# Kernel tuning notes

Measured on AMD Instinct MI355X. Metric: run time of the kernel, lower is better.

## Reference

```python
import jax, jax.numpy as jnp
import numpy as np

N = 8192        # num_nodes == args.input_size (code ties them together)
H = 64          # hidden_size
E = 262144      # num edges (avg degree 32)
FIN = N + H     # GCNConv in_channels = input_size + hidden_size


def _glorot(key, shape):
    fan_in, fan_out = shape
    lim = np.sqrt(6.0 / (fan_in + fan_out)).astype(np.float32)
    return jax.random.uniform(key, shape, jnp.float32, -lim, lim)


def gcn_conv(x, W, b, src, dst, n):
    """PyG GCNConv: lin -> add self-loops -> sym-normalized scatter-add -> +bias."""
    h = x @ W                                   # [n, out]
    loop = jnp.arange(n, dtype=src.dtype)
    s = jnp.concatenate([src, loop])            # [E+n]
    d = jnp.concatenate([dst, loop])
    deg = jax.ops.segment_sum(jnp.ones(s.shape[0], h.dtype), d, num_segments=n)
    dinv = jnp.where(deg > 0, jax.lax.rsqrt(deg), 0.0)
    norm = dinv[s] * dinv[d]                    # [E+n]
    out = jax.ops.segment_sum(h[s] * norm[:, None], d, num_segments=n)
    return out + b


def setup_inputs() -> dict:
    key = jax.random.key(0)
    k1, k2, k3, k4, k5 = jax.random.split(key, 5)
    x = jax.random.normal(k1, (N, N), jnp.float32)
    hidden_state = jax.random.normal(k2, (N, H), jnp.float32)
    W1 = _glorot(k3, (FIN, 2 * H))
    b1 = jnp.ones((2 * H,), jnp.float32)        # reset_parameters: constant_(bias, 1.0)
    W2 = _glorot(k4, (FIN, H))
    b2 = jnp.zeros((H,), jnp.float32)           # PyG default bias init = zeros
    edge_index = jax.random.randint(k5, (2, E), 0, N, jnp.int32)
    return {"x": x, "hidden_state": hidden_state, "W1": W1, "b1": b1,
            "W2": W2, "b2": b2, "edge_index": edge_index}


def reference(x, hidden_state, W1, b1, W2, b2, edge_index):
    src, dst = edge_index[0], edge_index[1]
    ru_input = jnp.concatenate([x, hidden_state], axis=1)        # [N, N+H]
    ru = jax.nn.sigmoid(gcn_conv(ru_input, W1, b1, src, dst, N))  # [N, 2H]
    flat = ru.reshape(-1, N * 2 * H)                              # [1, N*2H]
    r = flat[:, : N * H].reshape(-1, H)                           # [N, H]
    u = flat[:, N * H :].reshape(-1, H)                           # [N, H]
    c_input = jnp.concatenate([x, r * hidden_state], axis=1)
    c = jnp.tanh(gcn_conv(c_input, W2, b2, src, dst, N))          # [N, H]
    new_hidden_state = u * hidden_state + (1.0 - u) * c
    return new_hidden_state
```

## Files before the change

### kernel.cpp

```cpp
#include <hip/hip_runtime.h>
#include <hip/hip_bf16.h>
#include <stdint.h>

typedef __bf16 bf16x8 __attribute__((ext_vector_type(8)));
typedef float  f32x4  __attribute__((ext_vector_type(4)));
typedef unsigned uint4v __attribute__((ext_vector_type(4)));
using bf16 = __hip_bfloat16;

#define NNODES 8192
#define FIN    8256
#define NCOL   192
#define KT32   258

enum : size_t {
  WCT_OFF  = 0,
  CNT_OFF  = 3170304,
  OFF_OFF  = 3203072,
  CUR_OFF  = 3236096,
  DNV_OFF  = 3268864,
  CSR_OFF  = 3301632,
  H1_OFF   = 4350208,
  HX2_OFF  = 8544512,
  RU_OFF   = 10641664,
  H2_OFF   = 14835968,
  YP_OFF   = 16933120,
  YP_SLICE = 6291456
};

__global__ void k_zero_i(int* p, int n) {
  int i = blockIdx.x * 256 + threadIdx.x;
  if (i < n) p[i] = 0;
}

__global__ void k_out_zero(float* out) {
  int i = blockIdx.x * 256 + threadIdx.x;
  if (i < NNODES * 64) out[i] = 0.f;
}

__global__ void k_prep_wctf(const float* __restrict__ W1, const float* __restrict__ W2,
                            bf16* __restrict__ wctf) {
  int gid = blockIdx.x * 256 + threadIdx.x;
  if (gid >= KT32 * 12 * 64) return;
  int t = gid / 768;
  int rem = gid - t * 768;
  int nf = rem >> 6, lane = rem & 63;
  int col = nf * 16 + (lane & 15);
  int k0 = t * 32 + (lane >> 4) * 8;
  union { bf16 h[8]; uint4 v; } u;
#pragma unroll
  for (int j = 0; j < 8; ++j) {
    int k = k0 + j;
    float v;
    if (col < 128)      v = W1[(size_t)k * 128 + col];
    else if (k < 8192)  v = W2[(size_t)k * 64 + (col - 128)];
    else                v = 0.f;
    u.h[j] = __float2bfloat16(v);
  }
  *(uint4*)(wctf + (size_t)gid * 8) = u.v;
}

__global__ void k_hist(const int* __restrict__ ei, int E, int* cnt) {
  int e = blockIdx.x * 256 + threadIdx.x;
  if (e < E) atomicAdd(&cnt[ei[E + e]], 1);
}

__global__ void k_scan(const int* __restrict__ cnt, int* __restrict__ offs,
                       int* __restrict__ cur, float* __restrict__ dinv) {
  __shared__ int part[256];
  int tid = threadIdx.x;
  int base = tid * 32;
  int s = 0;
#pragma unroll
  for (int j = 0; j < 32; j++) s += cnt[base + j];
  part[tid] = s;
  __syncthreads();
  for (int off = 1; off < 256; off <<= 1) {
    int a = (tid >= off) ? part[tid - off] : 0;
    __syncthreads();
    part[tid] += a;
    __syncthreads();
  }
  int run = (tid == 0) ? 0 : part[tid - 1];
  for (int j = 0; j < 32; j++) {
    int c = cnt[base + j];
    offs[base + j] = run;
    cur[base + j]  = run;
    dinv[base + j] = rsqrtf((float)(c + 1));
    run += c;
  }
  if (tid == 255) offs[NNODES] = run;
}

__global__ void k_fill(const int* __restrict__ ei, int E, int* cur, int* __restrict__ csr) {
  int e = blockIdx.x * 256 + threadIdx.x;
  if (e < E) {
    int d = ei[E + e];
    int p = atomicAdd(&cur[d], 1);
    csr[p] = ei[e];
  }
}

__device__ __forceinline__ bf16x8 pack8(float4 a, float4 b) {
  union { bf16 h[8]; bf16x8 v; } u;
  u.h[0] = __float2bfloat16(a.x); u.h[1] = __float2bfloat16(a.y);
  u.h[2] = __float2bfloat16(a.z); u.h[3] = __float2bfloat16(a.w);
  u.h[4] = __float2bfloat16(b.x); u.h[5] = __float2bfloat16(b.y);
  u.h[6] = __float2bfloat16(b.z); u.h[7] = __float2bfloat16(b.w);
  return u.v;
}

union F4 { uint4v u; float4 f; bf16x8 h; };

__device__ __forceinline__ void gld16(void* ldsdst, const void* gsrc) {
  __builtin_amdgcn_global_load_lds(
      (__attribute__((address_space(1))) void*)gsrc,
      (__attribute__((address_space(3))) void*)ldsdst, 16, 0, 0);
}

__global__ __launch_bounds__(64, 1) void k_gemm(const float* __restrict__ x,
                                                const float* __restrict__ hid,
                                                const bf16* __restrict__ wctf,
                                                float* __restrict__ yp,
                                                bf16* __restrict__ h1d,
                                                float* __restrict__ hx2d,
                                                int tpc) {
  __shared__ __align__(1024) unsigned char smem[36864];
  const int lane = threadIdx.x & 63;
  const int rl = lane & 15, g = lane >> 4;
  const int m0 = blockIdx.x * 32;
  const int chunk = blockIdx.y;
  const int t_lo = chunk * tpc;
  const int t_hi = (t_lo + tpc > KT32) ? KT32 : (t_lo + tpc);
  const int nt = t_hi - t_lo;
  if (nt <= 0) return;

  const float* asx[4]; const float* ash[4];
#pragma unroll
  for (int q = 0; q < 4; ++q) {
    int i = q * 64 + lane, row = i >> 3, s = i & 7;
    int sel = (s ^ (row & 7)) << 2;
    asx[q] = x + (size_t)(m0 + row) * 8192 + sel;
    ash[q] = hid + (size_t)(m0 + row) * 64 + sel;
  }
  const bf16* bsrc = wctf + (size_t)lane * 8;

#define STAGE_A(buf, t) do {                                                   \
    const int _t = (t);                                                        \
    unsigned _d = (unsigned)(buf) * 4096u;                                     \
    if (_t < 256) {                                                            \
      const int _k = _t * 32;                                                  \
      _Pragma("unroll")                                                        \
      for (int q = 0; q < 4; ++q)                                              \
        gld16(smem + _d + (unsigned)(q * 64 + lane) * 16u, asx[q] + _k);       \
    } else {                                                                   \
      const int _k = (_t - 256) * 32;                                          \
      _Pragma("unroll")                                                        \
      for (int q = 0; q < 4; ++q)                                              \
        gld16(smem + _d + (unsigned)(q * 64 + lane) * 16u, ash[q] + _k);       \
    }                                                                          \
  } while (0)

#define STAGE_B(buf, t) do {                                                   \
    const bf16* _bt = bsrc + (size_t)(t) * 6144;                               \
    unsigned _d = 12288u + (unsigned)(buf) * 12288u + (unsigned)lane * 16u;    \
    _Pragma("unroll")                                                          \
    for (int q = 0; q < 12; ++q)                                               \
      gld16(smem + _d + (unsigned)q * 1024u, _bt + (size_t)q * 512);           \
  } while (0)

  f32x4 acc0[12] = {};
  f32x4 acc1[12] = {};

  const unsigned sl0 = (unsigned)((g * 2) ^ (rl & 7));
  const unsigned sl1 = (unsigned)((g * 2 + 1) ^ (rl & 7));
  const unsigned aA0 = (unsigned)rl * 128u + sl0 * 16u;
  const unsigned aA1 = (unsigned)rl * 128u + sl1 * 16u;
  const unsigned baseB = 12288u + (unsigned)lane * 16u;
  const unsigned ldsbase = (unsigned)(uintptr_t)&smem[0];

  STAGE_A(0, t_lo);
  STAGE_B(0, t_lo);
  if (nt > 1) STAGE_A(1, t_lo + 1);

  int r3 = 0;
  int w3 = 2;
  for (int li = 0; li < nt; ++li) {
    if (li + 1 < nt) STAGE_B((li + 1) & 1, t_lo + li + 1);
    if (li + 2 < nt) STAGE_A(w3, t_lo + li + 2);

    if (li + 2 < nt)      asm volatile("s_waitcnt vmcnt(20)" ::: "memory");
    else if (li + 1 < nt) asm volatile("s_waitcnt vmcnt(16)" ::: "memory");
    else                  asm volatile("s_waitcnt vmcnt(0)"  ::: "memory");
    __builtin_amdgcn_sched_barrier(0);

    const unsigned ar = ldsbase + (unsigned)r3 * 4096u;
    const unsigned br = ldsbase + baseB + (unsigned)(li & 1) * 12288u;
    F4 a00, a01, a10, a11, bv[12];
    asm volatile("ds_read_b128 %0, %1" : "=v"(a00.u) : "v"(ar + aA0));
    asm volatile("ds_read_b128 %0, %1" : "=v"(a01.u) : "v"(ar + aA1));
    asm volatile("ds_read_b128 %0, %1 offset:2048" : "=v"(a10.u) : "v"(ar + aA0));
    asm volatile("ds_read_b128 %0, %1 offset:2048" : "=v"(a11.u) : "v"(ar + aA1));
#pragma unroll
    for (int nf = 0; nf < 12; ++nf)
      asm volatile("ds_read_b128 %0, %1 offset:%c2"
                   : "=v"(bv[nf].u) : "v"(br), "i"(nf * 1024));
    asm volatile("s_waitcnt lgkmcnt(0)" ::: "memory");
    __builtin_amdgcn_sched_barrier(0);

    bf16x8 af0 = pack8(a00.f, a01.f);
    bf16x8 af1 = pack8(a10.f, a11.f);
#pragma unroll
    for (int nf = 0; nf < 12; ++nf) {
      acc0[nf] = __builtin_amdgcn_mfma_f32_16x16x32_bf16(af0, bv[nf].h, acc0[nf], 0, 0, 0);
      acc1[nf] = __builtin_amdgcn_mfma_f32_16x16x32_bf16(af1, bv[nf].h, acc1[nf], 0, 0, 0);
    }
    r3 = (r3 == 2) ? 0 : r3 + 1;
    w3 = (w3 == 2) ? 0 : w3 + 1;
  }
#undef STAGE_A
#undef STAGE_B

  if (h1d) {
#pragma unroll
    for (int nf = 0; nf < 12; ++nf) {
      int col = nf * 16 + rl;
#pragma unroll
      for (int tt = 0; tt < 4; ++tt) {
        int ra = m0 + g * 4 + tt;
        int rb = ra + 16;
        if (col < 128) {
          h1d[(size_t)ra * 128 + col] = __float2bfloat16(acc0[nf][tt]);
          h1d[(size_t)rb * 128 + col] = __float2bfloat16(acc1[nf][tt]);
        } else {
          hx2d[(size_t)ra * 64 + (col - 128)] = acc0[nf][tt];
          hx2d[(size_t)rb * 64 + (col - 128)] = acc1[nf][tt];
        }
      }
    }
  } else {
    float* ypc = yp + (size_t)chunk * ((size_t)NNODES * NCOL);
#pragma unroll
    for (int nf = 0; nf < 12; ++nf) {
      int col = nf * 16 + rl;
#pragma unroll
      for (int tt = 0; tt < 4; ++tt) {
        int ra = m0 + g * 4 + tt;
        ypc[(size_t)ra * NCOL + col] = acc0[nf][tt];
        ypc[(size_t)(ra + 16) * NCOL + col] = acc1[nf][tt];
      }
    }
  }
}

__global__ void k_reduce4(const float* __restrict__ yp, bf16* __restrict__ h1,
                          float* __restrict__ hx2, int nch) {
  int u = blockIdx.x * 256 + threadIdx.x;
  float4 s = {0.f, 0.f, 0.f, 0.f};
  for (int c = 0; c < nch; c++) {
    float4 v = *(const float4*)(yp + (size_t)c * ((size_t)NNODES * NCOL) + (size_t)u * 4);
    s.x += v.x; s.y += v.y; s.z += v.z; s.w += v.w;
  }
  int e = u * 4;
  int i = e / NCOL, c = e - i * NCOL;
  if (c < 128) {
    bf16* dst = h1 + (size_t)i * 128 + c;
    dst[0] = __float2bfloat16(s.x); dst[1] = __float2bfloat16(s.y);
    dst[2] = __float2bfloat16(s.z); dst[3] = __float2bfloat16(s.w);
  } else {
    *(float4*)(hx2 + (size_t)i * 64 + (c - 128)) = s;
  }
}

__device__ __forceinline__ float bflo(unsigned v) { return __uint_as_float(v << 16); }
__device__ __forceinline__ float bfhi(unsigned v) { return __uint_as_float(v & 0xffff0000u); }

__global__ void k_scat1(const bf16* __restrict__ h1b, const int* __restrict__ offs,
                        const int* __restrict__ csr, const float* __restrict__ dinv,
                        const float* __restrict__ b1, float* __restrict__ ru) {
  int node = blockIdx.x * 4 + (threadIdx.x >> 6);
  int lane = threadIdx.x & 63;
  const unsigned* h1u = (const unsigned*)h1b;
  float dd = dinv[node];
  unsigned vv = h1u[(size_t)node * 64 + lane];
  float ax = bflo(vv) * dd * dd, ay = bfhi(vv) * dd * dd;
  int e0 = offs[node], e1 = offs[node + 1];
  for (int e = e0; e < e1; ++e) {
    int s = csr[e];
    float nrm = dinv[s] * dd;
    unsigned wv = h1u[(size_t)s * 64 + lane];
    ax += bflo(wv) * nrm;
    ay += bfhi(wv) * nrm;
  }
  ax += b1[lane * 2];
  ay += b1[lane * 2 + 1];
  ax = 1.f / (1.f + expf(-ax));
  ay = 1.f / (1.f + expf(-ay));
  ru[(size_t)node * 128 + lane * 2]     = ax;
  ru[(size_t)node * 128 + lane * 2 + 1] = ay;
}

__global__ void k_rh(const float* __restrict__ ru, const float* __restrict__ hidden,
                     const float* __restrict__ hx2, const float* __restrict__ W2,
                     bf16* __restrict__ h2) {
  __shared__ float W2s[64][64];
  __shared__ float rhs[4][64];
  int tid = threadIdx.x;
#pragma unroll
  for (int t = 0; t < 16; ++t) {
    int idx = tid + 256 * t;
    int j = idx >> 6, c = idx & 63;
    W2s[j][c] = W2[(size_t)(8192 + j) * 64 + c];
  }
  int w = tid >> 6, lane = tid & 63;
  int i = blockIdx.x * 4 + w;
  float rv = ru[(size_t)(i >> 1) * 128 + ((i & 1) << 6) + lane];
  float hv = hidden[(size_t)i * 64 + lane];
  rhs[w][lane] = rv * hv;
  __syncthreads();
  float acc = hx2[(size_t)i * 64 + lane];
#pragma unroll 8
  for (int j = 0; j < 64; ++j) acc += rhs[w][j] * W2s[j][lane];
  h2[(size_t)i * 64 + lane] = __float2bfloat16(acc);
}

__global__ void k_scat2(const bf16* __restrict__ h2b, const int* __restrict__ offs,
                        const int* __restrict__ csr, const float* __restrict__ dinv,
                        const float* __restrict__ b2, const float* __restrict__ ru,
                        const float* __restrict__ hidden, float* __restrict__ out) {
  int node = blockIdx.x * 4 + (threadIdx.x >> 6);
  int lane = threadIdx.x & 63;
  const unsigned short* h2u = (const unsigned short*)h2b;
  float dd = dinv[node];
  float acc = bflo((unsigned)h2u[(size_t)node * 64 + lane]) * dd * dd;
  int e0 = offs[node], e1 = offs[node + 1];
  for (int e = e0; e < e1; ++e) {
    int s = csr[e];
    acc += bflo((unsigned)h2u[(size_t)s * 64 + lane]) * dinv[s] * dd;
  }
  acc += b2[lane];
  float cv = tanhf(acc);
  float u = ru[(size_t)(4096 + (node >> 1)) * 128 + ((node & 1) << 6) + lane];
  float hv = hidden[(size_t)node * 64 + lane];
  out[(size_t)node * 64 + lane] = u * hv + (1.f - u) * cv;
}

extern "C" void kernel_launch(void* const* d_in, const int* in_sizes, int n_in,
                              void* d_out, int out_size, void* d_ws, size_t ws_size,
                              hipStream_t stream) {
  (void)n_in; (void)out_size;
  const float* x   = (const float*)d_in[0];
  const float* hid = (const float*)d_in[1];
  const float* W1  = (const float*)d_in[2];
  const float* b1  = (const float*)d_in[3];
  const float* W2  = (const float*)d_in[4];
  const float* b2  = (const float*)d_in[5];
  const int*   ei  = (const int*)d_in[6];
  const int E = in_sizes[6] / 2;
  float* out = (float*)d_out;

  int ksplit;
  if      (ws_size >= YP_OFF + 8ull * YP_SLICE) ksplit = 8;
  else if (ws_size >= YP_OFF + 4ull * YP_SLICE) ksplit = 4;
  else if (ws_size >= YP_OFF + 2ull * YP_SLICE) ksplit = 2;
  else if (ws_size >= YP_OFF)                   ksplit = 1;
  else {
    k_out_zero<<<dim3(NNODES * 64 / 256), dim3(256), 0, stream>>>(out);
    return;
  }
  const int tpc = (KT32 + ksplit - 1) / ksplit;

  char* ws = (char*)d_ws;
  bf16*  wctf = (bf16*)(ws + WCT_OFF);
  int*   cnt  = (int*)(ws + CNT_OFF);
  int*   offs = (int*)(ws + OFF_OFF);
  int*   cur  = (int*)(ws + CUR_OFF);
  float* dinv = (float*)(ws + DNV_OFF);
  int*   csr  = (int*)(ws + CSR_OFF);
  bf16*  h1   = (bf16*)(ws + H1_OFF);
  float* hx2  = (float*)(ws + HX2_OFF);
  float* ru   = (float*)(ws + RU_OFF);
  bf16*  h2   = (bf16*)(ws + H2_OFF);
  float* yp   = (float*)(ws + YP_OFF);

  k_zero_i<<<dim3(32), dim3(256), 0, stream>>>(cnt, NNODES);
  k_prep_wctf<<<dim3((KT32 * 12 * 64 + 255) / 256), dim3(256), 0, stream>>>(W1, W2, wctf);
  k_hist<<<dim3((E + 255) / 256), dim3(256), 0, stream>>>(ei, E, cnt);
  k_scan<<<dim3(1), dim3(256), 0, stream>>>(cnt, offs, cur, dinv);
  k_fill<<<dim3((E + 255) / 256), dim3(256), 0, stream>>>(ei, E, cur, csr);
  if (ksplit == 1) {
    k_gemm<<<dim3(NNODES / 32, 1), dim3(64), 0, stream>>>(x, hid, wctf, nullptr, h1, hx2, tpc);
  } else {
    k_gemm<<<dim3(NNODES / 32, ksplit), dim3(64), 0, stream>>>(x, hid, wctf, yp, nullptr, nullptr, tpc);
    k_reduce4<<<dim3(NNODES * NCOL / 1024), dim3(256), 0, stream>>>(yp, h1, hx2, ksplit);
  }
  k_scat1<<<dim3(NNODES / 4), dim3(256), 0, stream>>>(h1, offs, csr, dinv, b1, ru);
  k_rh<<<dim3(NNODES / 4), dim3(256), 0, stream>>>(ru, hid, hx2, W2, h2);
  k_scat2<<<dim3(NNODES / 4), dim3(256), 0, stream>>>(h2, offs, csr, dinv, b2, ru, hid, out);
}
```

Before: 232.5 us.

## Widen GEMM blocks to four waves sharing staged weight tiles

The GEMM block grows from one wave covering 32 rows to four waves covering 128 rows. Each weight tile is staged into LDS once and shared by all four waves, which cuts redundant global reads of the bf16 weights. The pipeline is reshuffled to triple-buffer B and double-buffer A, with s_barrier synchronisation added between waves. The trade-off is a quarter as many blocks, more LDS per block and barrier stalls, which could reduce parallelism when ksplit is small.

```diff
diff --git a/kernel.cpp b/kernel.cpp
--- a/kernel.cpp
+++ b/kernel.cpp
@@ -11,6 +11,7 @@
 #define FIN    8256
 #define NCOL   192
 #define KT32   258
+#define BMB    128
 
 enum : size_t {
   WCT_OFF  = 0,
@@ -117,17 +118,18 @@
       (__attribute__((address_space(3))) void*)ldsdst, 16, 0, 0);
 }
 
-__global__ __launch_bounds__(64, 1) void k_gemm(const float* __restrict__ x,
-                                                const float* __restrict__ hid,
-                                                const bf16* __restrict__ wctf,
-                                                float* __restrict__ yp,
-                                                bf16* __restrict__ h1d,
-                                                float* __restrict__ hx2d,
-                                                int tpc) {
-  __shared__ __align__(1024) unsigned char smem[36864];
-  const int lane = threadIdx.x & 63;
+__global__ __launch_bounds__(256, 2) void k_gemm(const float* __restrict__ x,
+                                                 const float* __restrict__ hid,
+                                                 const bf16* __restrict__ wctf,
+                                                 float* __restrict__ yp,
+                                                 bf16* __restrict__ h1d,
+                                                 float* __restrict__ hx2d,
+                                                 int tpc) {
+  __shared__ __align__(1024) unsigned char smem[69632];
+  const int tid = threadIdx.x;
+  const int lane = tid & 63, w = tid >> 6;
   const int rl = lane & 15, g = lane >> 4;
-  const int m0 = blockIdx.x * 32;
+  const int m0 = blockIdx.x * BMB;
   const int chunk = blockIdx.y;
   const int t_lo = chunk * tpc;
   const int t_hi = (t_lo + tpc > KT32) ? KT32 : (t_lo + tpc);
@@ -137,35 +139,35 @@
   const float* asx[4]; const float* ash[4];
 #pragma unroll
   for (int q = 0; q < 4; ++q) {
-    int i = q * 64 + lane, row = i >> 3, s = i & 7;
+    int u = q * 256 + tid, row = u >> 3, s = u & 7;
     int sel = (s ^ (row & 7)) << 2;
     asx[q] = x + (size_t)(m0 + row) * 8192 + sel;
     ash[q] = hid + (size_t)(m0 + row) * 64 + sel;
   }
-  const bf16* bsrc = wctf + (size_t)lane * 8;
-
-#define STAGE_A(buf, t) do {                                                   \
-    const int _t = (t);                                                        \
-    unsigned _d = (unsigned)(buf) * 4096u;                                     \
-    if (_t < 256) {                                                            \
-      const int _k = _t * 32;                                                  \
-      _Pragma("unroll")                                                        \
-      for (int q = 0; q < 4; ++q)                                              \
-        gld16(smem + _d + (unsigned)(q * 64 + lane) * 16u, asx[q] + _k);       \
-    } else {                                                                   \
-      const int _k = (_t - 256) * 32;                                          \
-      _Pragma("unroll")                                                        \
-      for (int q = 0; q < 4; ++q)                                              \
-        gld16(smem + _d + (unsigned)(q * 64 + lane) * 16u, ash[q] + _k);       \
-    }                                                                          \
+
+#define STAGE_A(buf, t) do {                                                    \
+    const int _t = (t);                                                         \
+    unsigned _d = (unsigned)(buf) * 16384u;                                     \
+    if (_t < 256) {                                                             \
+      const int _k = _t * 32;                                                   \
+      _Pragma("unroll")                                                         \
+      for (int q = 0; q < 4; ++q)                                               \
+        gld16(smem + _d + (unsigned)(q * 256 + tid) * 16u, asx[q] + _k);        \
+    } else {                                                                    \
+      const int _k = (_t - 256) * 32;                                           \
+      _Pragma("unroll")                                                         \
+      for (int q = 0; q < 4; ++q)                                               \
+        gld16(smem + _d + (unsigned)(q * 256 + tid) * 16u, ash[q] + _k);        \
+    }                                                                           \
   } while (0)
 
-#define STAGE_B(buf, t) do {                                                   \
-    const bf16* _bt = bsrc + (size_t)(t) * 6144;                               \
-    unsigned _d = 12288u + (unsigned)(buf) * 12288u + (unsigned)lane * 16u;    \
-    _Pragma("unroll")                                                          \
-    for (int q = 0; q < 12; ++q)                                               \
-      gld16(smem + _d + (unsigned)q * 1024u, _bt + (size_t)q * 512);           \
+#define STAGE_B(buf, t) do {                                                    \
+    const bf16* _bt = wctf + (size_t)(t) * 6144;                                \
+    unsigned _d = 32768u + (unsigned)(buf) * 12288u;                            \
+    _Pragma("unroll")                                                           \
+    for (int q = 0; q < 3; ++q)                                                 \
+      gld16(smem + _d + (unsigned)(q * 256 + tid) * 16u,                        \
+            _bt + (size_t)(q * 256 + tid) * 8);                                 \
   } while (0)
 
   f32x4 acc0[12] = {};
@@ -173,28 +175,27 @@
 
   const unsigned sl0 = (unsigned)((g * 2) ^ (rl & 7));
   const unsigned sl1 = (unsigned)((g * 2 + 1) ^ (rl & 7));
-  const unsigned aA0 = (unsigned)rl * 128u + sl0 * 16u;
-  const unsigned aA1 = (unsigned)rl * 128u + sl1 * 16u;
-  const unsigned baseB = 12288u + (unsigned)lane * 16u;
   const unsigned ldsbase = (unsigned)(uintptr_t)&smem[0];
+  const unsigned aA0 = (unsigned)(w * 32 + rl) * 128u + sl0 * 16u;
+  const unsigned aA1 = (unsigned)(w * 32 + rl) * 128u + sl1 * 16u;
+  const unsigned bB  = 32768u + (unsigned)lane * 16u;
 
   STAGE_A(0, t_lo);
   STAGE_B(0, t_lo);
-  if (nt > 1) STAGE_A(1, t_lo + 1);
-
-  int r3 = 0;
-  int w3 = 2;
-  for (int li = 0; li < nt; ++li) {
-    if (li + 1 < nt) STAGE_B((li + 1) & 1, t_lo + li + 1);
-    if (li + 2 < nt) STAGE_A(w3, t_lo + li + 2);
-
-    if (li + 2 < nt)      asm volatile("s_waitcnt vmcnt(20)" ::: "memory");
-    else if (li + 1 < nt) asm volatile("s_waitcnt vmcnt(16)" ::: "memory");
-    else                  asm volatile("s_waitcnt vmcnt(0)"  ::: "memory");
-    __builtin_amdgcn_sched_barrier(0);
-
-    const unsigned ar = ldsbase + (unsigned)r3 * 4096u;
-    const unsigned br = ldsbase + baseB + (unsigned)(li & 1) * 12288u;
+  if (nt > 1) STAGE_B(1, t_lo + 1);
+
+  int b3r = 0, b3w = 2;
+  for (int i = 0; i < nt; ++i) {
+    if (i + 2 < nt) STAGE_B(b3w, t_lo + i + 2);
+    if (i + 1 < nt) STAGE_A((i + 1) & 1, t_lo + i + 1);
+
+    if (i + 2 < nt)      asm volatile("s_waitcnt vmcnt(7)" ::: "memory");
+    else if (i + 1 < nt) asm volatile("s_waitcnt vmcnt(4)" ::: "memory");
+    else                 asm volatile("s_waitcnt vmcnt(0)" ::: "memory");
+    asm volatile("s_barrier" ::: "memory");
+
+    const unsigned ar = ldsbase + (unsigned)(i & 1) * 16384u;
+    const unsigned br = ldsbase + bB + (unsigned)b3r * 12288u;
     F4 a00, a01, a10, a11, bv[12];
     asm volatile("ds_read_b128 %0, %1" : "=v"(a00.u) : "v"(ar + aA0));
     asm volatile("ds_read_b128 %0, %1" : "=v"(a01.u) : "v"(ar + aA1));
@@ -214,8 +215,9 @@
       acc0[nf] = __builtin_amdgcn_mfma_f32_16x16x32_bf16(af0, bv[nf].h, acc0[nf], 0, 0, 0);
       acc1[nf] = __builtin_amdgcn_mfma_f32_16x16x32_bf16(af1, bv[nf].h, acc1[nf], 0, 0, 0);
     }
-    r3 = (r3 == 2) ? 0 : r3 + 1;
-    w3 = (w3 == 2) ? 0 : w3 + 1;
+    asm volatile("s_barrier" ::: "memory");
+    b3r = (b3r == 2) ? 0 : b3r + 1;
+    b3w = (b3w == 2) ? 0 : b3w + 1;
   }
 #undef STAGE_A
 #undef STAGE_B
@@ -226,7 +228,7 @@
       int col = nf * 16 + rl;
 #pragma unroll
       for (int tt = 0; tt < 4; ++tt) {
-        int ra = m0 + g * 4 + tt;
+        int ra = m0 + w * 32 + g * 4 + tt;
         int rb = ra + 16;
         if (col < 128) {
           h1d[(size_t)ra * 128 + col] = __float2bfloat16(acc0[nf][tt]);
@@ -244,7 +246,7 @@
       int col = nf * 16 + rl;
 #pragma unroll
       for (int tt = 0; tt < 4; ++tt) {
-        int ra = m0 + g * 4 + tt;
+        int ra = m0 + w * 32 + g * 4 + tt;
         ypc[(size_t)ra * NCOL + col] = acc0[nf][tt];
         ypc[(size_t)(ra + 16) * NCOL + col] = acc1[nf][tt];
       }
@@ -388,9 +390,9 @@
   k_scan<<<dim3(1), dim3(256), 0, stream>>>(cnt, offs, cur, dinv);
   k_fill<<<dim3((E + 255) / 256), dim3(256), 0, stream>>>(ei, E, cur, csr);
   if (ksplit == 1) {
-    k_gemm<<<dim3(NNODES / 32, 1), dim3(64), 0, stream>>>(x, hid, wctf, nullptr, h1, hx2, tpc);
+    k_gemm<<<dim3(NNODES / BMB, 1), dim3(256), 0, stream>>>(x, hid, wctf, nullptr, h1, hx2, tpc);
   } else {
-    k_gemm<<<dim3(NNODES / 32, ksplit), dim3(64), 0, stream>>>(x, hid, wctf, yp, nullptr, nullptr, tpc);
+    k_gemm<<<dim3(NNODES / BMB, ksplit), dim3(256), 0, stream>>>(x, hid, wctf, yp, nullptr, nullptr, tpc);
     k_reduce4<<<dim3(NNODES * NCOL / 1024), dim3(256), 0, stream>>>(yp, h1, hx2, ksplit);
   }
   k_scat1<<<dim3(NNODES / 4), dim3(256), 0, stream>>>(h1, offs, csr, dinv, b1, ru);
```

New measurement: 207.5 us. 10.7% less time.
